# Performance work log

Measured on AMD Instinct MI355X. Metric: run time of the kernel, lower is better.

## Reference

```python
import jax, jax.numpy as jnp
import numpy as np

N = 50000   # nodes
E = 800000  # edges
D = 128     # hidden_dim
LN_EPS = 1e-5


def _mlp2(x, W1, b1, W2, b2, act_last):
    y = jax.nn.silu(x @ W1 + b1)
    y = y @ W2 + b2
    return jax.nn.silu(y) if act_last else y


def setup_inputs() -> dict:
    key = jax.random.key(0)
    ks = jax.random.split(key, 20)
    s = 1.0 / np.sqrt(D)
    inp = {
        "h": jax.random.normal(ks[0], (N, D), jnp.float32),
        "x": jax.random.normal(ks[1], (N, 3), jnp.float32),
        "vel_all": jax.random.normal(ks[2], (N, 5, 3), jnp.float32),
        "edge_index": jax.random.randint(ks[3], (2, E), 0, N, jnp.int64),
        # phi_e: Linear(2D+11, D) -> SiLU -> Linear(D, D) -> SiLU   (weights stored [in,out])
        "We1": jax.random.uniform(ks[4], (2 * D + 11, D), jnp.float32, -s, s),
        "be1": jax.random.uniform(ks[5], (D,), jnp.float32, -s, s),
        "We2": jax.random.uniform(ks[6], (D, D), jnp.float32, -s, s),
        "be2": jax.random.uniform(ks[7], (D,), jnp.float32, -s, s),
        # phi_x: Linear(D, D) -> SiLU -> Linear(D, 1)
        "Wx1": jax.random.uniform(ks[8], (D, D), jnp.float32, -s, s),
        "bx1": jax.random.uniform(ks[9], (D,), jnp.float32, -s, s),
        "Wx2": jax.random.uniform(ks[10], (D, 1), jnp.float32, -s, s),
        "bx2": jax.random.uniform(ks[11], (1,), jnp.float32, -s, s),
        # phi_h: Linear(2D, D) -> SiLU -> Linear(D, D)
        "Wh1": jax.random.uniform(ks[12], (2 * D, D), jnp.float32, -s, s),
        "bh1": jax.random.uniform(ks[13], (D,), jnp.float32, -s, s),
        "Wh2": jax.random.uniform(ks[14], (D, D), jnp.float32, -s, s),
        "bh2": jax.random.uniform(ks[15], (D,), jnp.float32, -s, s),
        # LayerNorm(D)
        "gamma": jnp.ones((D,), jnp.float32),
        "beta": jnp.zeros((D,), jnp.float32),
    }
    return inp


def reference(h, x, vel_all, edge_index, We1, be1, We2, be2, Wx1, bx1, Wx2, bx2,
              Wh1, bh1, Wh2, bh2, gamma, beta):
    n = h.shape[0]
    src, dst = edge_index[0], edge_index[1]

    rel = x[src] - x[dst]                                  # [E,3]
    dist2 = jnp.sum(rel * rel, axis=-1, keepdims=True)     # [E,1]
    dist = jnp.maximum(jnp.sqrt(dist2), 1e-8)
    r_hat = rel / dist                                     # [E,3]

    vel_proj_src = jnp.sum(vel_all[src] * r_hat[:, None, :], axis=-1)  # [E,5]
    vel_proj_dst = jnp.sum(vel_all[dst] * r_hat[:, None, :], axis=-1)  # [E,5]

    feat = jnp.concatenate([h[src], h[dst], dist2, vel_proj_src, vel_proj_dst], axis=-1)
    m_ij = _mlp2(feat, We1, be1, We2, be2, act_last=True)  # [E,D]

    # update_coords=True: scatter_mean of rel * phi_x(m_ij)
    coord_w = _mlp2(m_ij, Wx1, bx1, Wx2, bx2, act_last=False)          # [E,1]
    num = jax.ops.segment_sum(rel * coord_w, dst, num_segments=n)      # [N,3]
    cnt = jax.ops.segment_sum(jnp.ones((rel.shape[0], 1), x.dtype), dst, num_segments=n)
    delta_x = num / jnp.maximum(cnt, 1.0)
    x = x + delta_x

    agg = jax.ops.segment_sum(m_ij, dst, num_segments=n)               # [N,D]
    dh = _mlp2(jnp.concatenate([h, agg], axis=-1), Wh1, bh1, Wh2, bh2, act_last=False)
    h = h + dh  # dropout=0 -> identity

    # LayerNorm
    mu = jnp.mean(h, axis=-1, keepdims=True)
    var = jnp.mean(jnp.square(h - mu), axis=-1, keepdims=True)
    h = (h - mu) * jax.lax.rsqrt(var + LN_EPS) * gamma + beta

    return (h, x, m_ij)
```

## Files before the change

kernel.cpp:

```cpp
#include <hip/hip_runtime.h>
#include <stdint.h>

typedef __attribute__((ext_vector_type(8))) short bf16x8;
typedef __attribute__((ext_vector_type(4))) float f32x4;

__device__ __forceinline__ float bf2f(unsigned short u){
  union { unsigned int i; float f; } v; v.i = ((unsigned int)u) << 16; return v.f;
}
__device__ __forceinline__ unsigned short f2bf(float f){
  union { float f; unsigned int i; } v; v.f = f;
  unsigned int x = v.i;
  unsigned int r = (x + 0x7FFFu + ((x >> 16) & 1u)) >> 16;
  return (unsigned short)r;
}
__device__ __forceinline__ float silu_f(float v){
  return v / (1.0f + __expf(-v));
}

template<bool F32> __device__ __forceinline__ float ldv(const void* p, size_t i){
  if (F32) return ((const float*)p)[i];
  return bf2f(((const unsigned short*)p)[i]);
}
template<bool F32> __device__ __forceinline__ void stv(void* p, size_t i, float v){
  if (F32) ((float*)p)[i] = v;
  else     ((unsigned short*)p)[i] = f2bf(v);
}
template<bool I64> __device__ __forceinline__ int ldidx(const int* p, size_t i){
  return I64 ? p[2*i] : p[i];
}

__global__ void detect_kernel(const unsigned int* gw, const int* eidx, int N, int* flags){
  int f = 0;
  if (gw[0] == 0x3F800000u) f |= 1;
  bool i64 = true;
  for (int k = 0; k < 4; k++){
    int lo = eidx[2*k], hi = eidx[2*k+1];
    if (hi != 0 || lo < 0 || lo >= N) i64 = false;
  }
  if (i64) f |= 2;
  flags[0] = f;
}

struct __align__(16) NodePreSmem { float hlt[128][36]; };

template<bool F32>
__device__ void node_pre_impl(NodePreSmem& S, const void* h, const void* We1,
                              unsigned short* H1a, unsigned short* H1b, int N)
{
  const int t = threadIdx.x;
  const int base = blockIdx.x * 32;
  for (int i = t; i < 32*128; i += 256){
    int nl = i >> 7, j = i & 127;
    int node = base + nl;
    S.hlt[j][nl] = (node < N) ? ldv<F32>(h, (size_t)node*128 + j) : 0.0f;
  }
  __syncthreads();
  const int j = t & 127, half = t >> 7;
  const size_t wbase = (size_t)(half * 128) * 128;
  unsigned short* O = half ? H1b : H1a;
  float acc[32];
  #pragma unroll
  for (int nl=0; nl<32; nl++) acc[nl] = 0.0f;
  for (int k=0; k<128; k++){
    float w = ldv<F32>(We1, wbase + (size_t)k*128 + j);
    const float4* row = (const float4*)&S.hlt[k][0];
    #pragma unroll
    for (int g=0; g<8; g++){
      float4 hv = row[g];
      acc[g*4+0] += hv.x * w;
      acc[g*4+1] += hv.y * w;
      acc[g*4+2] += hv.z * w;
      acc[g*4+3] += hv.w * w;
    }
  }
  #pragma unroll
  for (int nl=0; nl<32; nl++){
    int node = base + nl;
    if (node < N) O[(size_t)node*128 + j] = f2bf(acc[nl]);
  }
}

__global__ __launch_bounds__(256) void node_pre(
    const void* h, const void* We1, unsigned short* H1a, unsigned short* H1b,
    int N, const int* flags)
{
  __shared__ NodePreSmem S;
  if (flags[0] & 1) node_pre_impl<true >(S, h, We1, H1a, H1b, N);
  else              node_pre_impl<false>(S, h, We1, H1a, H1b, N);
}

struct __align__(16) EdgeSmem {
  unsigned short m1s[64][136];
  unsigned short m2s[64][136];
  float rels[64][3];
  float geos[64][11];
  int   dsts[64];
  int   srcs[64];
  float wpart[4][64];
};

template<bool F32, bool I64>
__device__ void edge_impl(EdgeSmem& S,
    const void* xu, const void* velu, const int* eidx,
    const unsigned short* __restrict__ H1a, const unsigned short* __restrict__ H1b,
    const void* We1, const void* be1, const void* We2, const void* be2,
    const void* Wx1, const void* bx1, const void* Wx2, const void* bx2,
    void* out, size_t moff,
    float* __restrict__ agg, float* __restrict__ num, float* __restrict__ cnt,
    int N, int E, int ntiles)
{
  const int t = threadIdx.x;
  const int wave = t >> 6, lane = t & 63;
  const int col = lane & 15, quad = lane >> 4;
  const int colbase = wave * 32;

  bf16x8 bwe2[2][4], bwx1[2][4];
  float wx2v[2], be2v[2], bx1v[2];
  #pragma unroll
  for (int nt=0; nt<2; nt++){
    int n = colbase + nt*16 + col;
    wx2v[nt] = ldv<F32>(Wx2, n);
    be2v[nt] = ldv<F32>(be2, n);
    bx1v[nt] = ldv<F32>(bx1, n);
    #pragma unroll
    for (int kb=0; kb<4; kb++){
      bf16x8 a, b;
      #pragma unroll
      for (int jj=0; jj<8; jj++){
        int k = kb*32 + quad*8 + jj;
        a[jj] = (short)f2bf(ldv<F32>(We2, (size_t)k*128 + n));
        b[jj] = (short)f2bf(ldv<F32>(Wx1, (size_t)k*128 + n));
      }
      bwe2[nt][kb] = a; bwx1[nt][kb] = b;
    }
  }
  const int jfix = t & 127;
  float gw[11];
  #pragma unroll
  for (int k=0; k<11; k++) gw[k] = ldv<F32>(We1, (size_t)(256+k)*128 + jfix);
  const float be1j = ldv<F32>(be1, jfix);
  const float bx2v = ldv<F32>(bx2, 0);

  for (int tile = blockIdx.x; tile < ntiles; tile += gridDim.x){
    const int ebase = tile * 64;
    if (t < 64){
      int e = ebase + t;
      int s = 0, d = 0;
      if (e < E){ s = ldidx<I64>(eidx, e); d = ldidx<I64>(eidx, (size_t)E + e); }
      s = min(max(s, 0), N-1);
      d = min(max(d, 0), N-1);
      S.srcs[t] = s; S.dsts[t] = d;
      float rx = ldv<F32>(xu, s*3+0) - ldv<F32>(xu, d*3+0);
      float ry = ldv<F32>(xu, s*3+1) - ldv<F32>(xu, d*3+1);
      float rz = ldv<F32>(xu, s*3+2) - ldv<F32>(xu, d*3+2);
      float dist2 = rx*rx + ry*ry + rz*rz;
      float dist = fmaxf(sqrtf(dist2), 1e-8f);
      float inv = 1.0f / dist;
      float ux = rx*inv, uy = ry*inv, uz = rz*inv;
      S.rels[t][0]=rx; S.rels[t][1]=ry; S.rels[t][2]=rz;
      S.geos[t][0] = dist2;
      #pragma unroll
      for (int v=0; v<5; v++){
        S.geos[t][1+v] = ldv<F32>(velu, s*15+v*3+0)*ux + ldv<F32>(velu, s*15+v*3+1)*uy + ldv<F32>(velu, s*15+v*3+2)*uz;
        S.geos[t][6+v] = ldv<F32>(velu, d*15+v*3+0)*ux + ldv<F32>(velu, d*15+v*3+1)*uy + ldv<F32>(velu, d*15+v*3+2)*uz;
      }
    }
    __syncthreads();
    #pragma unroll
    for (int it=0; it<32; it++){
      int el = (t + it*256) >> 7;
      int s = S.srcs[el], d = S.dsts[el];
      float acc = bf2f(H1a[(size_t)s*128 + jfix]) + bf2f(H1b[(size_t)d*128 + jfix]) + be1j;
      #pragma unroll
      for (int k=0; k<11; k++) acc += gw[k] * S.geos[el][k];
      S.m1s[el][jfix] = f2bf(silu_f(acc));
    }
    __syncthreads();
    #pragma unroll
    for (int et=0; et<4; et++){
      #pragma unroll
      for (int nt=0; nt<2; nt++){
        f32x4 acc = { be2v[nt], be2v[nt], be2v[nt], be2v[nt] };
        #pragma unroll
        for (int kb=0; kb<4; kb++){
          bf16x8 a = *(const bf16x8*)&S.m1s[et*16 + col][kb*32 + quad*8];
          acc = __builtin_amdgcn_mfma_f32_16x16x32_bf16(a, bwe2[nt][kb], acc, 0, 0, 0);
        }
        int n = colbase + nt*16 + col;
        #pragma unroll
        for (int r=0; r<4; r++)
          S.m2s[et*16 + quad*4 + r][n] = f2bf(silu_f(acc[r]));
      }
    }
    __syncthreads();
    #pragma unroll
    for (int it=0; it<32; it++){
      int el = (t + it*256) >> 7;
      int e = ebase + el;
      if (e < E){
        float v = bf2f(S.m2s[el][jfix]);
        stv<F32>(out, moff + (size_t)e*128 + jfix, v);
        atomicAdd(&agg[(size_t)S.dsts[el]*128 + jfix], v);
      }
    }
    float part[4][4];
    #pragma unroll
    for (int et=0; et<4; et++)
      #pragma unroll
      for (int r=0; r<4; r++) part[et][r] = 0.0f;
    #pragma unroll
    for (int et=0; et<4; et++){
      #pragma unroll
      for (int nt=0; nt<2; nt++){
        f32x4 acc = { bx1v[nt], bx1v[nt], bx1v[nt], bx1v[nt] };
        #pragma unroll
        for (int kb=0; kb<4; kb++){
          bf16x8 a = *(const bf16x8*)&S.m2s[et*16 + col][kb*32 + quad*8];
          acc = __builtin_amdgcn_mfma_f32_16x16x32_bf16(a, bwx1[nt][kb], acc, 0, 0, 0);
        }
        #pragma unroll
        for (int r=0; r<4; r++) part[et][r] += silu_f(acc[r]) * wx2v[nt];
      }
    }
    #pragma unroll
    for (int et=0; et<4; et++){
      #pragma unroll
      for (int r=0; r<4; r++){
        float v = part[et][r];
        v += __shfl_xor(v, 1, 16);
        v += __shfl_xor(v, 2, 16);
        v += __shfl_xor(v, 4, 16);
        v += __shfl_xor(v, 8, 16);
        part[et][r] = v;
      }
    }
    if (col == 0){
      #pragma unroll
      for (int et=0; et<4; et++)
        #pragma unroll
        for (int r=0; r<4; r++)
          S.wpart[wave][et*16 + quad*4 + r] = part[et][r];
    }
    __syncthreads();
    if (t < 64){
      int e = ebase + t;
      if (e < E){
        float w = S.wpart[0][t] + S.wpart[1][t] + S.wpart[2][t] + S.wpart[3][t] + bx2v;
        int d = S.dsts[t];
        atomicAdd(&num[(size_t)d*3+0], S.rels[t][0]*w);
        atomicAdd(&num[(size_t)d*3+1], S.rels[t][1]*w);
        atomicAdd(&num[(size_t)d*3+2], S.rels[t][2]*w);
        atomicAdd(&cnt[d], 1.0f);
      }
    }
    __syncthreads();
  }
}

__global__ __launch_bounds__(256) void edge_kernel(
    const void* xu, const void* velu, const int* eidx,
    const unsigned short* H1a, const unsigned short* H1b,
    const void* We1, const void* be1, const void* We2, const void* be2,
    const void* Wx1, const void* bx1, const void* Wx2, const void* bx2,
    void* out, size_t moff, float* agg, float* num, float* cnt,
    int N, int E, int ntiles, const int* flags)
{
  __shared__ EdgeSmem S;
  int f = flags[0];
  if      (f == 0) edge_impl<false,false>(S, xu, velu, eidx, H1a, H1b, We1, be1, We2, be2, Wx1, bx1, Wx2, bx2, out, moff, agg, num, cnt, N, E, ntiles);
  else if (f == 1) edge_impl<true ,false>(S, xu, velu, eidx, H1a, H1b, We1, be1, We2, be2, Wx1, bx1, Wx2, bx2, out, moff, agg, num, cnt, N, E, ntiles);
  else if (f == 2) edge_impl<false,true >(S, xu, velu, eidx, H1a, H1b, We1, be1, We2, be2, Wx1, bx1, Wx2, bx2, out, moff, agg, num, cnt, N, E, ntiles);
  else             edge_impl<true ,true >(S, xu, velu, eidx, H1a, H1b, We1, be1, We2, be2, Wx1, bx1, Wx2, bx2, out, moff, agg, num, cnt, N, E, ntiles);
}

struct __align__(16) NodeFinalSmem {
  unsigned short ins[16][256];
  unsigned short y1s[16][128];
  float hns[16][128];
};

template<bool F32>
__device__ void node_final_impl(NodeFinalSmem& S,
    const void* h, const void* xu,
    const float* __restrict__ agg, const float* __restrict__ num, const float* __restrict__ cnt,
    const void* Wh1, const void* bh1, const void* Wh2, const void* bh2,
    const void* gam, const void* bet,
    void* out, size_t xoff, int N)
{
  const int t = threadIdx.x;
  const int base = blockIdx.x * 16;
  for (int i = t; i < 16*256; i += 256){
    int n = i >> 8, c = i & 255;
    int node = base + n;
    unsigned short v = 0;
    if (node < N){
      if (c < 128) v = f2bf(ldv<F32>(h, (size_t)node*128 + c));
      else         v = f2bf(agg[(size_t)node*128 + (c-128)]);
    }
    S.ins[n][c] = v;
  }
  __syncthreads();
  const int j = t & 127, nh = t >> 7;
  {
    float acc[8];
    #pragma unroll
    for (int u=0; u<8; u++) acc[u] = ldv<F32>(bh1, j);
    for (int k=0; k<256; k++){
      float w = ldv<F32>(Wh1, (size_t)k*128 + j);
      #pragma unroll
      for (int u=0; u<8; u++) acc[u] += bf2f(S.ins[nh + 2*u][k]) * w;
    }
    #pragma unroll
    for (int u=0; u<8; u++) S.y1s[nh + 2*u][j] = f2bf(silu_f(acc[u]));
  }
  __syncthreads();
  {
    float acc[8];
    #pragma unroll
    for (int u=0; u<8; u++) acc[u] = ldv<F32>(bh2, j);
    for (int k=0; k<128; k++){
      float w = ldv<F32>(Wh2, (size_t)k*128 + j);
      #pragma unroll
      for (int u=0; u<8; u++) acc[u] += bf2f(S.y1s[nh + 2*u][k]) * w;
    }
    #pragma unroll
    for (int u=0; u<8; u++){
      int n = nh + 2*u;
      int node = base + n;
      float hv = (node < N) ? ldv<F32>(h, (size_t)node*128 + j) : 0.0f;
      S.hns[n][j] = hv + acc[u];
    }
  }
  __syncthreads();
  {
    int n = t >> 4, sub = t & 15;
    float s = 0.0f, ss = 0.0f;
    #pragma unroll
    for (int i2=0; i2<8; i2++){
      float v = S.hns[n][sub + 16*i2];
      s += v; ss += v*v;
    }
    #pragma unroll
    for (int m=1; m<16; m<<=1){ s += __shfl_xor(s, m, 16); ss += __shfl_xor(ss, m, 16); }
    float mu = s * (1.0f/128.0f);
    float var = fmaxf(ss * (1.0f/128.0f) - mu*mu, 0.0f);
    float rs = rsqrtf(var + 1e-5f);
    int gnode = base + n;
    if (gnode < N){
      #pragma unroll
      for (int i2=0; i2<8; i2++){
        int jj = sub + 16*i2;
        float v = (S.hns[n][jj] - mu) * rs * ldv<F32>(gam, jj) + ldv<F32>(bet, jj);
        stv<F32>(out, (size_t)gnode*128 + jj, v);
      }
    }
  }
  if (t < 48){
    int n = t / 3, c = t % 3;
    int node = base + n;
    if (node < N){
      float cv = fmaxf(cnt[node], 1.0f);
      float dx = num[(size_t)node*3 + c] / cv;
      stv<F32>(out, xoff + (size_t)node*3 + c, ldv<F32>(xu, (size_t)node*3 + c) + dx);
    }
  }
}

__global__ __launch_bounds__(256) void node_final(
    const void* h, const void* xu,
    const float* agg, const float* num, const float* cnt,
    const void* Wh1, const void* bh1, const void* Wh2, const void* bh2,
    const void* gam, const void* bet,
    void* out, size_t xoff, int N, const int* flags)
{
  __shared__ NodeFinalSmem S;
  if (flags[0] & 1) node_final_impl<true >(S, h, xu, agg, num, cnt, Wh1, bh1, Wh2, bh2, gam, bet, out, xoff, N);
  else              node_final_impl<false>(S, h, xu, agg, num, cnt, Wh1, bh1, Wh2, bh2, gam, bet, out, xoff, N);
}

extern "C" void kernel_launch(void* const* d_in, const int* in_sizes, int n_in,
                              void* d_out, int out_size, void* d_ws, size_t ws_size,
                              hipStream_t stream)
{
  const int N = in_sizes[0] / 128;
  const int E = in_sizes[3] / 2;

  char* ws = (char*)d_ws;
  int* flags = (int*)ws;
  unsigned short* H1a = (unsigned short*)(ws + 256);
  unsigned short* H1b = H1a + (size_t)N * 128;
  float* agg = (float*)(ws + 256 + (size_t)N * 128 * 2 * 2);
  float* num = agg + (size_t)N * 128;
  float* cnt = num + (size_t)N * 3;

  detect_kernel<<<1, 1, 0, stream>>>((const unsigned int*)d_in[16], (const int*)d_in[3], N, flags);

  size_t zbytes = (size_t)N*128*4 + (size_t)N*3*4 + (size_t)N*4;
  hipMemsetAsync((void*)agg, 0, zbytes, stream);

  node_pre<<<(N + 31) / 32, 256, 0, stream>>>(d_in[0], d_in[4], H1a, H1b, N, flags);

  size_t xoff = (size_t)N * 128;
  size_t moff = (size_t)N * 128 + (size_t)N * 3;
  int ntiles = (E + 63) / 64;
  edge_kernel<<<2500, 256, 0, stream>>>(d_in[1], d_in[2], (const int*)d_in[3], H1a, H1b,
                                        d_in[4], d_in[5], d_in[6], d_in[7],
                                        d_in[8], d_in[9], d_in[10], d_in[11],
                                        d_out, moff, agg, num, cnt, N, E, ntiles, flags);

  node_final<<<(N + 15) / 16, 256, 0, stream>>>(d_in[0], d_in[1], agg, num, cnt,
                                                d_in[12], d_in[13], d_in[14], d_in[15],
                                                d_in[16], d_in[17],
                                                d_out, xoff, N, flags);
}
```

Measured before the change: 1.482 ms.

## Replace per-edge agg atomics with dst-bucketed gather in node_final

Adds a histogram kernel that counts edges per destination and records up to 64 edge ids per node in a bucket table. The edge kernel then writes m_ij with vectorized float4 stores and only uses atomics for edges past the bucket capacity, and node_final gathers each node's messages from the m_ij output instead of reading an atomically accumulated buffer. The integer count also replaces the float count atomic. It also spreads the per-edge geometry work across all 256 threads and processes two hidden columns per thread in the first layer. This trades 128 float atomics per edge for an extra pass that rereads m_ij, plus an extra kernel and a larger workspace.

```diff
diff --git a/kernel.cpp b/kernel.cpp
--- a/kernel.cpp
+++ b/kernel.cpp
@@ -1,5 +1,7 @@
 #include <hip/hip_runtime.h>
 #include <stdint.h>
+
+#define CAPB 64
 
 typedef __attribute__((ext_vector_type(8))) short bf16x8;
 typedef __attribute__((ext_vector_type(4))) float f32x4;
@@ -39,6 +41,20 @@
   }
   if (i64) f |= 2;
   flags[0] = f;
+}
+
+__global__ __launch_bounds__(256) void hist_kernel(
+    const int* eidx, int* cnt_i, int* bucket, int* slot, int N, int E, const int* flags)
+{
+  int e = blockIdx.x * 256 + threadIdx.x;
+  if (e >= E) return;
+  int d;
+  if (flags[0] & 2) d = eidx[2*((size_t)E + e)];
+  else              d = eidx[(size_t)E + e];
+  d = min(max(d, 0), N-1);
+  int p = atomicAdd(&cnt_i[d], 1);
+  slot[e] = p;
+  if (p < CAPB) bucket[(size_t)d*CAPB + p] = e;
 }
 
 struct __align__(16) NodePreSmem { float hlt[128][36]; };
@@ -96,6 +112,7 @@
   float geos[64][11];
   int   dsts[64];
   int   srcs[64];
+  int   slot[64];
   float wpart[4][64];
 };
 
@@ -106,7 +123,8 @@
     const void* We1, const void* be1, const void* We2, const void* be2,
     const void* Wx1, const void* bx1, const void* Wx2, const void* bx2,
     void* out, size_t moff,
-    float* __restrict__ agg, float* __restrict__ num, float* __restrict__ cnt,
+    float* __restrict__ agg, float* __restrict__ num,
+    const int* __restrict__ slotp,
     int N, int E, int ntiles)
 {
   const int t = threadIdx.x;
@@ -134,46 +152,63 @@
       bwe2[nt][kb] = a; bwx1[nt][kb] = b;
     }
   }
+  const int j0 = 2*lane, j1 = 2*lane + 1;
+  float gw0[11], gw1[11];
+  #pragma unroll
+  for (int k=0; k<11; k++){
+    gw0[k] = ldv<F32>(We1, (size_t)(256+k)*128 + j0);
+    gw1[k] = ldv<F32>(We1, (size_t)(256+k)*128 + j1);
+  }
+  const float be10 = ldv<F32>(be1, j0);
+  const float be11 = ldv<F32>(be1, j1);
   const int jfix = t & 127;
-  float gw[11];
-  #pragma unroll
-  for (int k=0; k<11; k++) gw[k] = ldv<F32>(We1, (size_t)(256+k)*128 + jfix);
-  const float be1j = ldv<F32>(be1, jfix);
   const float bx2v = ldv<F32>(bx2, 0);
 
   for (int tile = blockIdx.x; tile < ntiles; tile += gridDim.x){
     const int ebase = tile * 64;
-    if (t < 64){
-      int e = ebase + t;
+    {
+      const int el = t >> 2, part = t & 3;
+      const int e = ebase + el;
       int s = 0, d = 0;
       if (e < E){ s = ldidx<I64>(eidx, e); d = ldidx<I64>(eidx, (size_t)E + e); }
       s = min(max(s, 0), N-1);
       d = min(max(d, 0), N-1);
-      S.srcs[t] = s; S.dsts[t] = d;
-      float rx = ldv<F32>(xu, s*3+0) - ldv<F32>(xu, d*3+0);
-      float ry = ldv<F32>(xu, s*3+1) - ldv<F32>(xu, d*3+1);
-      float rz = ldv<F32>(xu, s*3+2) - ldv<F32>(xu, d*3+2);
+      float rx = ldv<F32>(xu, (size_t)s*3+0) - ldv<F32>(xu, (size_t)d*3+0);
+      float ry = ldv<F32>(xu, (size_t)s*3+1) - ldv<F32>(xu, (size_t)d*3+1);
+      float rz = ldv<F32>(xu, (size_t)s*3+2) - ldv<F32>(xu, (size_t)d*3+2);
       float dist2 = rx*rx + ry*ry + rz*rz;
       float dist = fmaxf(sqrtf(dist2), 1e-8f);
       float inv = 1.0f / dist;
       float ux = rx*inv, uy = ry*inv, uz = rz*inv;
-      S.rels[t][0]=rx; S.rels[t][1]=ry; S.rels[t][2]=rz;
-      S.geos[t][0] = dist2;
-      #pragma unroll
-      for (int v=0; v<5; v++){
-        S.geos[t][1+v] = ldv<F32>(velu, s*15+v*3+0)*ux + ldv<F32>(velu, s*15+v*3+1)*uy + ldv<F32>(velu, s*15+v*3+2)*uz;
-        S.geos[t][6+v] = ldv<F32>(velu, d*15+v*3+0)*ux + ldv<F32>(velu, d*15+v*3+1)*uy + ldv<F32>(velu, d*15+v*3+2)*uz;
+      if (part == 0){
+        S.srcs[el] = s; S.dsts[el] = d;
+        S.slot[el] = (e < E) ? slotp[e] : 0;
+        S.rels[el][0]=rx; S.rels[el][1]=ry; S.rels[el][2]=rz;
+        S.geos[el][0] = dist2;
+      }
+      for (int v = part; v < 10; v += 4){
+        size_t bidx = (v < 5) ? ((size_t)s*15 + v*3) : ((size_t)d*15 + (v-5)*3);
+        float pr = ldv<F32>(velu, bidx+0)*ux + ldv<F32>(velu, bidx+1)*uy + ldv<F32>(velu, bidx+2)*uz;
+        S.geos[el][1+v] = pr;
       }
     }
     __syncthreads();
     #pragma unroll
-    for (int it=0; it<32; it++){
-      int el = (t + it*256) >> 7;
-      int s = S.srcs[el], d = S.dsts[el];
-      float acc = bf2f(H1a[(size_t)s*128 + jfix]) + bf2f(H1b[(size_t)d*128 + jfix]) + be1j;
-      #pragma unroll
-      for (int k=0; k<11; k++) acc += gw[k] * S.geos[el][k];
-      S.m1s[el][jfix] = f2bf(silu_f(acc));
+    for (int it=0; it<16; it++){
+      const int el = it*4 + wave;
+      const int s = S.srcs[el], d = S.dsts[el];
+      const unsigned int ua = *(const unsigned int*)&H1a[(size_t)s*128 + j0];
+      const unsigned int ub = *(const unsigned int*)&H1b[(size_t)d*128 + j0];
+      float a0 = bf2f((unsigned short)(ua & 0xFFFFu)) + bf2f((unsigned short)(ub & 0xFFFFu)) + be10;
+      float a1 = bf2f((unsigned short)(ua >> 16))     + bf2f((unsigned short)(ub >> 16))     + be11;
+      #pragma unroll
+      for (int k=0; k<11; k++){
+        float g = S.geos[el][k];
+        a0 += gw0[k] * g;
+        a1 += gw1[k] * g;
+      }
+      unsigned int pk = (unsigned int)f2bf(silu_f(a0)) | ((unsigned int)f2bf(silu_f(a1)) << 16);
+      *(unsigned int*)&S.m1s[el][j0] = pk;
     }
     __syncthreads();
     #pragma unroll
@@ -193,14 +228,39 @@
       }
     }
     __syncthreads();
-    #pragma unroll
-    for (int it=0; it<32; it++){
-      int el = (t + it*256) >> 7;
-      int e = ebase + el;
-      if (e < E){
-        float v = bf2f(S.m2s[el][jfix]);
-        stv<F32>(out, moff + (size_t)e*128 + jfix, v);
-        atomicAdd(&agg[(size_t)S.dsts[el]*128 + jfix], v);
+    if (F32){
+      #pragma unroll
+      for (int it=0; it<4; it++){
+        const int sl = t + it*256;
+        const int el = sl >> 4, i8 = sl & 15;
+        const int e = ebase + el;
+        if (e < E){
+          const bf16x8 mv = *(const bf16x8*)&S.m2s[el][i8*8];
+          float f[8];
+          #pragma unroll
+          for (int j=0; j<8; j++) f[j] = bf2f((unsigned short)mv[j]);
+          float* op = (float*)out + moff + (size_t)e*128 + i8*8;
+          float4 v0 = { f[0], f[1], f[2], f[3] };
+          float4 v1 = { f[4], f[5], f[6], f[7] };
+          *(float4*)op = v0;
+          *(float4*)(op + 4) = v1;
+          if (S.slot[el] >= CAPB){
+            float* ap = &agg[(size_t)S.dsts[el]*128 + i8*8];
+            #pragma unroll
+            for (int j=0; j<8; j++) atomicAdd(ap + j, f[j]);
+          }
+        }
+      }
+    } else {
+      #pragma unroll
+      for (int it=0; it<32; it++){
+        int el = (t + it*256) >> 7;
+        int e = ebase + el;
+        if (e < E){
+          float v = bf2f(S.m2s[el][jfix]);
+          stv<F32>(out, moff + (size_t)e*128 + jfix, v);
+          atomicAdd(&agg[(size_t)S.dsts[el]*128 + jfix], v);
+        }
       }
     }
     float part[4][4];
@@ -250,7 +310,6 @@
         atomicAdd(&num[(size_t)d*3+0], S.rels[t][0]*w);
         atomicAdd(&num[(size_t)d*3+1], S.rels[t][1]*w);
         atomicAdd(&num[(size_t)d*3+2], S.rels[t][2]*w);
-        atomicAdd(&cnt[d], 1.0f);
       }
     }
     __syncthreads();
@@ -262,15 +321,15 @@
     const unsigned short* H1a, const unsigned short* H1b,
     const void* We1, const void* be1, const void* We2, const void* be2,
     const void* Wx1, const void* bx1, const void* Wx2, const void* bx2,
-    void* out, size_t moff, float* agg, float* num, float* cnt,
+    void* out, size_t moff, float* agg, float* num, const int* slotp,
     int N, int E, int ntiles, const int* flags)
 {
   __shared__ EdgeSmem S;
   int f = flags[0];
-  if      (f == 0) edge_impl<false,false>(S, xu, velu, eidx, H1a, H1b, We1, be1, We2, be2, Wx1, bx1, Wx2, bx2, out, moff, agg, num, cnt, N, E, ntiles);
-  else if (f == 1) edge_impl<true ,false>(S, xu, velu, eidx, H1a, H1b, We1, be1, We2, be2, Wx1, bx1, Wx2, bx2, out, moff, agg, num, cnt, N, E, ntiles);
-  else if (f == 2) edge_impl<false,true >(S, xu, velu, eidx, H1a, H1b, We1, be1, We2, be2, Wx1, bx1, Wx2, bx2, out, moff, agg, num, cnt, N, E, ntiles);
-  else             edge_impl<true ,true >(S, xu, velu, eidx, H1a, H1b, We1, be1, We2, be2, Wx1, bx1, Wx2, bx2, out, moff, agg, num, cnt, N, E, ntiles);
+  if      (f == 0) edge_impl<false,false>(S, xu, velu, eidx, H1a, H1b, We1, be1, We2, be2, Wx1, bx1, Wx2, bx2, out, moff, agg, num, slotp, N, E, ntiles);
+  else if (f == 1) edge_impl<true ,false>(S, xu, velu, eidx, H1a, H1b, We1, be1, We2, be2, Wx1, bx1, Wx2, bx2, out, moff, agg, num, slotp, N, E, ntiles);
+  else if (f == 2) edge_impl<false,true >(S, xu, velu, eidx, H1a, H1b, We1, be1, We2, be2, Wx1, bx1, Wx2, bx2, out, moff, agg, num, slotp, N, E, ntiles);
+  else             edge_impl<true ,true >(S, xu, velu, eidx, H1a, H1b, We1, be1, We2, be2, Wx1, bx1, Wx2, bx2, out, moff, agg, num, slotp, N, E, ntiles);
 }
 
 struct __align__(16) NodeFinalSmem {
@@ -282,22 +341,49 @@
 template<bool F32>
 __device__ void node_final_impl(NodeFinalSmem& S,
     const void* h, const void* xu,
-    const float* __restrict__ agg, const float* __restrict__ num, const float* __restrict__ cnt,
+    const float* __restrict__ agg, const float* __restrict__ num,
+    const int* __restrict__ cnt_i, const int* __restrict__ bucket,
     const void* Wh1, const void* bh1, const void* Wh2, const void* bh2,
     const void* gam, const void* bet,
-    void* out, size_t xoff, int N)
+    void* out, size_t xoff, size_t moff, int N)
 {
   const int t = threadIdx.x;
   const int base = blockIdx.x * 16;
-  for (int i = t; i < 16*256; i += 256){
-    int n = i >> 8, c = i & 255;
+  for (int i = t; i < 16*128; i += 256){
+    int n = i >> 7, c = i & 127;
     int node = base + n;
-    unsigned short v = 0;
+    S.ins[n][c] = (node < N) ? f2bf(ldv<F32>(h, (size_t)node*128 + c)) : (unsigned short)0;
+  }
+  if (F32){
+    const int g = t >> 4, i8 = t & 15;
+    const int node = base + g;
+    float a[8] = {0,0,0,0,0,0,0,0};
     if (node < N){
-      if (c < 128) v = f2bf(ldv<F32>(h, (size_t)node*128 + c));
-      else         v = f2bf(agg[(size_t)node*128 + (c-128)]);
-    }
-    S.ins[n][c] = v;
+      int deg = cnt_i[node];
+      int kmax = min(deg, CAPB);
+      const float* mbase = (const float*)out + moff;
+      for (int k = 0; k < kmax; k++){
+        int e = bucket[(size_t)node*CAPB + k];
+        const float* rp = mbase + (size_t)e*128 + i8*8;
+        float4 v0 = *(const float4*)rp;
+        float4 v1 = *(const float4*)(rp + 4);
+        a[0]+=v0.x; a[1]+=v0.y; a[2]+=v0.z; a[3]+=v0.w;
+        a[4]+=v1.x; a[5]+=v1.y; a[6]+=v1.z; a[7]+=v1.w;
+      }
+      if (deg > CAPB){
+        const float* ap = &agg[(size_t)node*128 + i8*8];
+        #pragma unroll
+        for (int j=0; j<8; j++) a[j] += ap[j];
+      }
+    }
+    #pragma unroll
+    for (int j=0; j<8; j++) S.ins[g][128 + i8*8 + j] = f2bf(a[j]);
+  } else {
+    for (int i = t; i < 16*128; i += 256){
+      int n = i >> 7, c = i & 127;
+      int node = base + n;
+      S.ins[n][128 + c] = (node < N) ? f2bf(agg[(size_t)node*128 + c]) : (unsigned short)0;
+    }
   }
   __syncthreads();
   const int j = t & 127, nh = t >> 7;
@@ -359,7 +445,7 @@
     int n = t / 3, c = t % 3;
     int node = base + n;
     if (node < N){
-      float cv = fmaxf(cnt[node], 1.0f);
+      float cv = fmaxf((float)cnt_i[node], 1.0f);
       float dx = num[(size_t)node*3 + c] / cv;
       stv<F32>(out, xoff + (size_t)node*3 + c, ldv<F32>(xu, (size_t)node*3 + c) + dx);
     }
@@ -368,14 +454,14 @@
 
 __global__ __launch_bounds__(256) void node_final(
     const void* h, const void* xu,
-    const float* agg, const float* num, const float* cnt,
+    const float* agg, const float* num, const int* cnt_i, const int* bucket,
     const void* Wh1, const void* bh1, const void* Wh2, const void* bh2,
     const void* gam, const void* bet,
-    void* out, size_t xoff, int N, const int* flags)
+    void* out, size_t xoff, size_t moff, int N, const int* flags)
 {
   __shared__ NodeFinalSmem S;
-  if (flags[0] & 1) node_final_impl<true >(S, h, xu, agg, num, cnt, Wh1, bh1, Wh2, bh2, gam, bet, out, xoff, N);
-  else              node_final_impl<false>(S, h, xu, agg, num, cnt, Wh1, bh1, Wh2, bh2, gam, bet, out, xoff, N);
+  if (flags[0] & 1) node_final_impl<true >(S, h, xu, agg, num, cnt_i, bucket, Wh1, bh1, Wh2, bh2, gam, bet, out, xoff, moff, N);
+  else              node_final_impl<false>(S, h, xu, agg, num, cnt_i, bucket, Wh1, bh1, Wh2, bh2, gam, bet, out, xoff, moff, N);
 }
 
 extern "C" void kernel_launch(void* const* d_in, const int* in_sizes, int n_in,
@@ -389,14 +475,18 @@
   int* flags = (int*)ws;
   unsigned short* H1a = (unsigned short*)(ws + 256);
   unsigned short* H1b = H1a + (size_t)N * 128;
-  float* agg = (float*)(ws + 256 + (size_t)N * 128 * 2 * 2);
-  float* num = agg + (size_t)N * 128;
-  float* cnt = num + (size_t)N * 3;
+  float* agg   = (float*)(ws + 256 + (size_t)N * 128 * 2 * 2);
+  float* num   = agg + (size_t)N * 128;
+  int*   cnt_i = (int*)(num + (size_t)N * 3);
+  int*   bucket = cnt_i + N;
+  int*   slot   = bucket + (size_t)N * CAPB;
 
   detect_kernel<<<1, 1, 0, stream>>>((const unsigned int*)d_in[16], (const int*)d_in[3], N, flags);
 
-  size_t zbytes = (size_t)N*128*4 + (size_t)N*3*4 + (size_t)N*4;
+  size_t zbytes = ((size_t)N*128 + (size_t)N*3 + (size_t)N) * 4;
   hipMemsetAsync((void*)agg, 0, zbytes, stream);
+
+  hist_kernel<<<(E + 255) / 256, 256, 0, stream>>>((const int*)d_in[3], cnt_i, bucket, slot, N, E, flags);
 
   node_pre<<<(N + 31) / 32, 256, 0, stream>>>(d_in[0], d_in[4], H1a, H1b, N, flags);
 
@@ -406,10 +496,10 @@
   edge_kernel<<<2500, 256, 0, stream>>>(d_in[1], d_in[2], (const int*)d_in[3], H1a, H1b,
                                         d_in[4], d_in[5], d_in[6], d_in[7],
                                         d_in[8], d_in[9], d_in[10], d_in[11],
-                                        d_out, moff, agg, num, cnt, N, E, ntiles, flags);
-
-  node_final<<<(N + 15) / 16, 256, 0, stream>>>(d_in[0], d_in[1], agg, num, cnt,
+                                        d_out, moff, agg, num, slot, N, E, ntiles, flags);
+
+  node_final<<<(N + 15) / 16, 256, 0, stream>>>(d_in[0], d_in[1], agg, num, cnt_i, bucket,
                                                 d_in[12], d_in[13], d_in[14], d_in[15],
                                                 d_in[16], d_in[17],
-                                                d_out, xoff, N, flags);
-}
+                                                d_out, xoff, moff, N, flags);
+}
```

Result: no change. 1.502 ms (+1.3%).
